# Optimization experiments

Hardware: AMD Instinct MI355X
Metric: run time of the kernel (lower is better)

## Reference

```python
import jax, jax.numpy as jnp
import numpy as np

EMBED_DIM = 1024
NUM_HEADS = 16
D_K = EMBED_DIM // NUM_HEADS


def setup_inputs() -> dict:
    key = jax.random.key(0)
    kx, kq, kk, kv, ko = jax.random.split(key, 5)
    scale = 1.0 / np.sqrt(EMBED_DIM)
    return {
        "x": jax.random.normal(kx, (4, 2048, EMBED_DIM), dtype=jnp.float32),
        # nn.Linear weights are [out, in]; we store them the same way.
        "w_q": jax.random.normal(kq, (EMBED_DIM, EMBED_DIM), dtype=jnp.float32) * scale,
        "w_k": jax.random.normal(kk, (EMBED_DIM, EMBED_DIM), dtype=jnp.float32) * scale,
        "w_v": jax.random.normal(kv, (EMBED_DIM, EMBED_DIM), dtype=jnp.float32) * scale,
        "w_o": jax.random.normal(ko, (EMBED_DIM, EMBED_DIM), dtype=jnp.float32) * scale,
    }


def reference(x, w_q, w_k, w_v, w_o):
    B, S, E = x.shape
    H, Dk = NUM_HEADS, D_K

    def proj(w):  # [B,S,E] @ [E,E]^T -> [B,H,S,Dk]
        y = jnp.einsum('bse,fe->bsf', x, w)
        return y.reshape(B, S, H, Dk).transpose(0, 2, 1, 3)

    q, k, v = proj(w_q), proj(w_k), proj(w_v)
    scores = jnp.einsum('bhsd,bhtd->bhst', q, k) / jnp.sqrt(jnp.float32(Dk))
    attn = jax.nn.softmax(scores, axis=-1)  # dropout p=0 -> identity
    out = jnp.einsum('bhst,bhtd->bhsd', attn, v)
    out = out.transpose(0, 2, 1, 3).reshape(B, S, E)
    return jnp.einsum('bse,fe->bsf', out, w_o)
```

## Files before the change

### kernel.cpp

```cpp
#include <hip/hip_runtime.h>
#include <stdint.h>

typedef unsigned short u16;
typedef __attribute__((ext_vector_type(8))) short bf16x8;
typedef __attribute__((ext_vector_type(4))) float f32x4;
typedef __attribute__((ext_vector_type(16))) float f32x16;

#define EMB 1024
#define SLEN 2048
#define NHD 16
#define DKH 64

__device__ __forceinline__ u16 f2bf(float f) {
  uint32_t u = __float_as_uint(f);
  u = (u + 0x7fffu + ((u >> 16) & 1u)) >> 16;
  return (u16)u;
}

__device__ __forceinline__ void load_lds16(const void* g, void* l) {
  __builtin_amdgcn_global_load_lds(
      (const __attribute__((address_space(1))) uint32_t*)g,
      (__attribute__((address_space(3))) uint32_t*)l, 16, 0, 0);
}

__global__ __launch_bounds__(256) void cvt_f32_bf16(const float* __restrict__ in,
                                                    u16* __restrict__ out, int n4) {
  int i = blockIdx.x * 256 + threadIdx.x;
  if (i >= n4) return;
  float4 v = ((const float4*)in)[i];
  union { u16 h[4]; uint64_t q; } o;
  o.h[0] = f2bf(v.x); o.h[1] = f2bf(v.y); o.h[2] = f2bf(v.z); o.h[3] = f2bf(v.w);
  ((uint64_t*)out)[i] = o.q;
}

__global__ __launch_bounds__(256) void cvt_w4(
    const float* __restrict__ w0, const float* __restrict__ w1,
    const float* __restrict__ w2, const float* __restrict__ w3,
    u16* __restrict__ o0, u16* __restrict__ o1,
    u16* __restrict__ o2, u16* __restrict__ o3) {
  const float* in = (blockIdx.y == 0) ? w0 : (blockIdx.y == 1) ? w1
                    : (blockIdx.y == 2) ? w2 : w3;
  u16* out = (blockIdx.y == 0) ? o0 : (blockIdx.y == 1) ? o1
             : (blockIdx.y == 2) ? o2 : o3;
  int i = blockIdx.x * 256 + threadIdx.x;
  float4 v = ((const float4*)in)[i];
  union { u16 h[4]; uint64_t q; } o;
  o.h[0] = f2bf(v.x); o.h[1] = f2bf(v.y); o.h[2] = f2bf(v.z); o.h[3] = f2bf(v.w);
  ((uint64_t*)out)[i] = o.q;
}

template<int MODE>
__device__ __forceinline__ void gemm_body(const u16* __restrict__ A,
                                          const u16* __restrict__ W,
                                          void* __restrict__ C,
                                          int bm, int bn,
                                          u16* At, u16* Bt) {
  const int tid = threadIdx.x;
  const int l = tid & 63, w = tid >> 6;
  const int wm = w >> 1, wn = w & 1;
  const int lr = l & 15, lg = l >> 4;

  f32x4 acc[4][4] = {};

  const int e0 = w * 1024 + l * 8;
  const int r0 = e0 >> 5, c0 = e0 & 31;
  const int e1 = e0 + 512;
  const int r1 = e1 >> 5, c1 = e1 & 31;
  const u16* Ag0 = A + (size_t)(bm + r0) * EMB + c0;
  const u16* Ag1 = A + (size_t)(bm + r1) * EMB + c1;
  const u16* Wg0 = W + (size_t)(bn + r0) * EMB + c0;
  const u16* Wg1 = W + (size_t)(bn + r1) * EMB + c1;

  auto stage = [&](int buf, int k0) {
    load_lds16(Ag0 + k0, At + buf * 4096 + w * 1024);
    load_lds16(Ag1 + k0, At + buf * 4096 + w * 1024 + 512);
    load_lds16(Wg0 + k0, Bt + buf * 4096 + w * 1024);
    load_lds16(Wg1 + k0, Bt + buf * 4096 + w * 1024 + 512);
  };

  stage(0, 0);
  stage(1, 32);
  int cur = 0;

#pragma unroll 1
  for (int it = 0; it < 32; ++it) {
    if (it < 31)
      asm volatile("s_waitcnt vmcnt(4)" ::: "memory");
    else
      asm volatile("s_waitcnt vmcnt(0)" ::: "memory");
    __builtin_amdgcn_s_barrier();
    if (it < 30) {
      int nb = cur + 2; if (nb >= 3) nb -= 3;
      stage(nb, (it + 2) * 32);
    }
    bf16x8 af[4], bf[4];
#pragma unroll
    for (int i = 0; i < 4; ++i)
      af[i] = *(const bf16x8*)(At + cur * 4096 + (wm * 64 + i * 16 + lr) * 32 + lg * 8);
#pragma unroll
    for (int j = 0; j < 4; ++j)
      bf[j] = *(const bf16x8*)(Bt + cur * 4096 + (wn * 64 + j * 16 + lr) * 32 + lg * 8);
    __builtin_amdgcn_s_setprio(1);
#pragma unroll
    for (int i = 0; i < 4; ++i)
#pragma unroll
      for (int j = 0; j < 4; ++j)
        acc[i][j] = __builtin_amdgcn_mfma_f32_16x16x32_bf16(af[i], bf[j], acc[i][j], 0, 0, 0);
    __builtin_amdgcn_s_setprio(0);
    ++cur; if (cur == 3) cur = 0;
  }

  if (MODE == 2) {
#pragma unroll
    for (int i = 0; i < 4; ++i) {
      const int m0 = bm + wm * 64 + i * 16 + lg * 4;
      const int bb = m0 >> 11;
      const int ss = m0 & 2047;
#pragma unroll
      for (int j = 0; j < 4; ++j) {
        const int n = bn + wn * 64 + j * 16 + lr;
        const int hh = n >> 6, dd = n & 63;
        union { u16 h[4]; uint64_t q; } pk;
#pragma unroll
        for (int r = 0; r < 4; ++r) pk.h[r] = f2bf(acc[i][j][r]);
        *(uint64_t*)((u16*)C + ((size_t)((bb * 16 + hh) * 64 + dd)) * 2048 + ss) = pk.q;
      }
    }
  } else {
#pragma unroll
    for (int i = 0; i < 4; ++i) {
      const int mb = bm + wm * 64 + i * 16 + lg * 4;
#pragma unroll
      for (int j = 0; j < 4; ++j) {
        const int col = bn + wn * 64 + j * 16 + lr;
#pragma unroll
        for (int r = 0; r < 4; ++r) {
          float v = acc[i][j][r];
          if (MODE == 1) v *= 0.18033688011112042f;
          if (MODE == 3)
            ((float*)C)[(size_t)(mb + r) * EMB + col] = v;
          else
            ((u16*)C)[(size_t)(mb + r) * EMB + col] = f2bf(v);
        }
      }
    }
  }
}

__global__ __launch_bounds__(256) void gemm_qkv(
    const u16* __restrict__ A,
    const u16* __restrict__ wq, const u16* __restrict__ wk, const u16* __restrict__ wv,
    u16* __restrict__ Qo, u16* __restrict__ Ko, u16* __restrict__ Vo) {
  __shared__ __align__(16) u16 At[3 * 4096];
  __shared__ __align__(16) u16 Bt[3 * 4096];
  const int bid = blockIdx.x;
  const int wgid = (bid & 7) * 192 + (bid >> 3);
  const int z = wgid >> 9;
  const int rem = wgid & 511;
  const int bm = (rem >> 3) * 128, bn = (rem & 7) * 128;
  if (z == 0) gemm_body<1>(A, wq, Qo, bm, bn, At, Bt);
  else if (z == 1) gemm_body<0>(A, wk, Ko, bm, bn, At, Bt);
  else gemm_body<2>(A, wv, Vo, bm, bn, At, Bt);
}

__global__ __launch_bounds__(256) void gemm_out(const u16* __restrict__ A,
                                                const u16* __restrict__ W,
                                                float* __restrict__ C) {
  __shared__ __align__(16) u16 At[3 * 4096];
  __shared__ __align__(16) u16 Bt[3 * 4096];
  const int bid = blockIdx.x;
  const int wgid = (bid & 7) * 64 + (bid >> 3);
  const int bm = (wgid >> 3) * 128, bn = (wgid & 7) * 128;
  gemm_body<3>(A, W, C, bm, bn, At, Bt);
}

__global__ __launch_bounds__(512, 4) void attn_fwd(const u16* __restrict__ Q,
                                                   const u16* __restrict__ K,
                                                   const u16* __restrict__ VT,
                                                   u16* __restrict__ O) {
  __shared__ __align__(16) u16 lds[3][2][64 * 64];
  const int tid = threadIdx.x;
  const int l = tid & 63, w = tid >> 6;
  const int ql = l & 31, hi = l >> 5;
  const int bid = blockIdx.x;
  const int bh = (bid & 7) * 8 + (bid >> 6);
  const int qt = (bid >> 3) & 7;
  const int b = bh >> 4, h = bh & 15;
  const int qw = qt * 256 + w * 32;
  const size_t qkb = ((size_t)b * SLEN) * EMB + h * DKH;
  const size_t vb = (size_t)bh * DKH * SLEN;

  const int srow = tid >> 3;
  const int scb = ((tid & 7) * 16) ^ ((srow & 7) << 4);
  const u16* Ksrc = K + qkb + (size_t)srow * EMB + (scb >> 1);
  const u16* Vsrc = VT + vb + (size_t)srow * SLEN + (scb >> 1);

  auto stage = [&](int buf, int t) {
    load_lds16(Ksrc + (size_t)t * 64 * EMB, (char*)(&lds[buf][0][0]) + w * 1024);
    load_lds16(Vsrc + t * 64, (char*)(&lds[buf][1][0]) + w * 1024);
  };

  bf16x8 qf[4];
#pragma unroll
  for (int ks = 0; ks < 4; ++ks)
    qf[ks] = *(const bf16x8*)(Q + qkb + (size_t)(qw + ql) * EMB + ks * 16 + hi * 8);

  f32x16 accd[2] = {};
  float lsum = 0.f;

  stage(0, 0);
  stage(1, 1);
  int cur = 0;
#pragma unroll 1
  for (int t = 0; t < 32; ++t) {
    if (t < 30) {
      int nb = cur + 2; if (nb >= 3) nb -= 3;
      stage(nb, t + 2);
      asm volatile("s_waitcnt vmcnt(4)" ::: "memory");
    } else if (t == 30) {
      asm volatile("s_waitcnt vmcnt(2)" ::: "memory");
    } else {
      asm volatile("s_waitcnt vmcnt(0)" ::: "memory");
    }
    __builtin_amdgcn_s_barrier();

    const u16* Kt = &lds[cur][0][0];
    const u16* Vt = &lds[cur][1][0];

    f32x16 sacc[2] = {};
    __builtin_amdgcn_s_setprio(1);
#pragma unroll
    for (int kf2 = 0; kf2 < 2; ++kf2) {
      const int row = kf2 * 32 + ql;
      const int swz = (row & 7) << 4;
#pragma unroll
      for (int ks = 0; ks < 4; ++ks) {
        bf16x8 kf = *(const bf16x8*)((const char*)Kt + row * 128 +
                                     ((ks * 32 + hi * 16) ^ swz));
        sacc[kf2] = __builtin_amdgcn_mfma_f32_32x32x16_bf16(kf, qf[ks], sacc[kf2], 0, 0, 0);
      }
    }
    __builtin_amdgcn_s_setprio(0);

#pragma unroll
    for (int kf2 = 0; kf2 < 2; ++kf2)
#pragma unroll
      for (int r = 0; r < 16; ++r)
        sacc[kf2][r] = __builtin_amdgcn_exp2f(sacc[kf2][r]);
    float ps[8];
#pragma unroll
    for (int g = 0; g < 8; ++g) {
      const int kf2 = g >> 2, r0 = (g & 3) * 4;
      ps[g] = (sacc[kf2][r0] + sacc[kf2][r0 + 1]) + (sacc[kf2][r0 + 2] + sacc[kf2][r0 + 3]);
    }
    lsum += ((ps[0] + ps[1]) + (ps[2] + ps[3])) + ((ps[4] + ps[5]) + (ps[6] + ps[7]));

    __builtin_amdgcn_s_setprio(1);
#pragma unroll
    for (int ks = 0; ks < 4; ++ks) {
      const int kf2 = ks >> 1;
      const int e0 = (ks & 1) * 8;
      uint32_t a0, a1, b0, b1;
      asm("v_cvt_pk_bf16_f32 %0, %1, %2" : "=v"(a0) : "v"(sacc[kf2][e0 + 0]), "v"(sacc[kf2][e0 + 1]));
      asm("v_cvt_pk_bf16_f32 %0, %1, %2" : "=v"(a1) : "v"(sacc[kf2][e0 + 2]), "v"(sacc[kf2][e0 + 3]));
      asm("v_cvt_pk_bf16_f32 %0, %1, %2" : "=v"(b0) : "v"(sacc[kf2][e0 + 4]), "v"(sacc[kf2][e0 + 5]));
      asm("v_cvt_pk_bf16_f32 %0, %1, %2" : "=v"(b1) : "v"(sacc[kf2][e0 + 6]), "v"(sacc[kf2][e0 + 7]));
      asm("v_permlane32_swap_b32 %0, %1" : "+v"(a0), "+v"(b0));
      asm("v_permlane32_swap_b32 %0, %1" : "+v"(a1), "+v"(b1));
      union { uint32_t d[4]; bf16x8 v; } pa;
      pa.d[0] = a0; pa.d[1] = a1; pa.d[2] = b0; pa.d[3] = b1;
#pragma unroll
      for (int df = 0; df < 2; ++df) {
        const int vr = df * 32 + ql;
        bf16x8 vf = *(const bf16x8*)((const char*)Vt + vr * 128 +
                                     ((ks * 32 + hi * 16) ^ ((vr & 7) << 4)));
        accd[df] = __builtin_amdgcn_mfma_f32_32x32x16_bf16(pa.v, vf, accd[df], 0, 0, 0);
      }
    }
    __builtin_amdgcn_s_setprio(0);
    __builtin_amdgcn_s_barrier();
    ++cur; if (cur == 3) cur = 0;
  }

  lsum += __shfl_xor(lsum, 32, 64);

  __syncthreads();
  u16* slice = &lds[0][0][0] + w * 2048;
#pragma unroll
  for (int reg = 0; reg < 16; ++reg) {
    const int rowq = (reg & 3) + 8 * (reg >> 2) + 4 * hi;
    const float li = 1.0f / __shfl(lsum, rowq, 64);
    slice[rowq * 64 + ql] = f2bf(accd[0][reg] * li);
    slice[rowq * 64 + 32 + ql] = f2bf(accd[1][reg] * li);
  }
  asm volatile("s_waitcnt lgkmcnt(0)" ::: "memory");
#pragma unroll
  for (int j = 0; j < 4; ++j) {
    const int byteoff = j * 1024 + l * 16;
    const int row = byteoff >> 7;
    const int colB = byteoff & 127;
    bf16x8 vv = *(const bf16x8*)((const char*)slice + byteoff);
    *(bf16x8*)(O + qkb + (size_t)(qw + row) * EMB + (colB >> 1)) = vv;
  }
}

extern "C" void kernel_launch(void* const* d_in, const int* in_sizes, int n_in,
                              void* d_out, int out_size, void* d_ws, size_t ws_size,
                              hipStream_t stream) {
  const float* x  = (const float*)d_in[0];
  const float* wq = (const float*)d_in[1];
  const float* wk = (const float*)d_in[2];
  const float* wv = (const float*)d_in[3];
  const float* wo = (const float*)d_in[4];

  char* ws = (char*)d_ws;
  u16* xb  = (u16*)(ws + 0);
  u16* wqb = (u16*)(ws + 16777216);
  u16* wkb = (u16*)(ws + 18874368);
  u16* wvb = (u16*)(ws + 20971520);
  u16* wob = (u16*)(ws + 23068672);
  u16* Qb  = (u16*)(ws + 25165824);
  u16* Kb  = (u16*)(ws + 41943040);
  u16* VTb = (u16*)(ws + 58720256);
  u16* AO  = (u16*)(ws + 75497472);

  cvt_f32_bf16<<<2097152 / 256, 256, 0, stream>>>(x, xb, 2097152);
  cvt_w4<<<dim3(262144 / 256, 4), 256, 0, stream>>>(wq, wk, wv, wo, wqb, wkb, wvb, wob);

  gemm_qkv<<<dim3(1536), 256, 0, stream>>>(xb, wqb, wkb, wvb, Qb, Kb, VTb);
  attn_fwd<<<dim3(512), 512, 0, stream>>>(Qb, Kb, VTb, AO);
  gemm_out<<<dim3(512), 256, 0, stream>>>(AO, wob, (float*)d_out);
}
```

Before: 178.3 us.

## Use 8 waves per GEMM tile and merge conversion kernels into one launch

The GEMM blocks grow from 256 to 512 threads. Each wave now computes a 64x32 sub-tile instead of 64x64, and the staging loads are split so each thread issues one A and one W load per stage. This halves the accumulator count per wave and doubles the number of waves available to hide latency, at the cost of less operand reuse per wave and more LDS reads in total. Separately, the x and weight fp32-to-bf16 conversions are fused into one kernel to drop a launch.

```diff
diff --git a/kernel.cpp b/kernel.cpp
--- a/kernel.cpp
+++ b/kernel.cpp
@@ -23,26 +23,25 @@
       (__attribute__((address_space(3))) uint32_t*)l, 16, 0, 0);
 }
 
-__global__ __launch_bounds__(256) void cvt_f32_bf16(const float* __restrict__ in,
-                                                    u16* __restrict__ out, int n4) {
-  int i = blockIdx.x * 256 + threadIdx.x;
-  if (i >= n4) return;
-  float4 v = ((const float4*)in)[i];
-  union { u16 h[4]; uint64_t q; } o;
-  o.h[0] = f2bf(v.x); o.h[1] = f2bf(v.y); o.h[2] = f2bf(v.z); o.h[3] = f2bf(v.w);
-  ((uint64_t*)out)[i] = o.q;
-}
-
-__global__ __launch_bounds__(256) void cvt_w4(
+__global__ __launch_bounds__(256) void cvt_all(
+    const float* __restrict__ x,
     const float* __restrict__ w0, const float* __restrict__ w1,
     const float* __restrict__ w2, const float* __restrict__ w3,
+    u16* __restrict__ xo,
     u16* __restrict__ o0, u16* __restrict__ o1,
     u16* __restrict__ o2, u16* __restrict__ o3) {
-  const float* in = (blockIdx.y == 0) ? w0 : (blockIdx.y == 1) ? w1
-                    : (blockIdx.y == 2) ? w2 : w3;
-  u16* out = (blockIdx.y == 0) ? o0 : (blockIdx.y == 1) ? o1
-             : (blockIdx.y == 2) ? o2 : o3;
-  int i = blockIdx.x * 256 + threadIdx.x;
+  const int bid = blockIdx.x;
+  const float* in;
+  u16* out;
+  int i;
+  if (bid < 8192) {
+    in = x; out = xo; i = bid * 256 + threadIdx.x;
+  } else {
+    const int ws = (bid - 8192) >> 10;
+    in  = (ws == 0) ? w0 : (ws == 1) ? w1 : (ws == 2) ? w2 : w3;
+    out = (ws == 0) ? o0 : (ws == 1) ? o1 : (ws == 2) ? o2 : o3;
+    i = ((bid - 8192) & 1023) * 256 + threadIdx.x;
+  }
   float4 v = ((const float4*)in)[i];
   union { u16 h[4]; uint64_t q; } o;
   o.h[0] = f2bf(v.x); o.h[1] = f2bf(v.y); o.h[2] = f2bf(v.z); o.h[3] = f2bf(v.w);
@@ -57,25 +56,19 @@
                                           u16* At, u16* Bt) {
   const int tid = threadIdx.x;
   const int l = tid & 63, w = tid >> 6;
-  const int wm = w >> 1, wn = w & 1;
+  const int wm = w >> 2, wn = w & 3;
   const int lr = l & 15, lg = l >> 4;
 
-  f32x4 acc[4][4] = {};
-
-  const int e0 = w * 1024 + l * 8;
-  const int r0 = e0 >> 5, c0 = e0 & 31;
-  const int e1 = e0 + 512;
-  const int r1 = e1 >> 5, c1 = e1 & 31;
-  const u16* Ag0 = A + (size_t)(bm + r0) * EMB + c0;
-  const u16* Ag1 = A + (size_t)(bm + r1) * EMB + c1;
-  const u16* Wg0 = W + (size_t)(bn + r0) * EMB + c0;
-  const u16* Wg1 = W + (size_t)(bn + r1) * EMB + c1;
+  f32x4 acc[4][2] = {};
+
+  const int sr = w * 16 + (l >> 2);
+  const int sc = (l & 3) * 8;
+  const u16* Ag = A + (size_t)(bm + sr) * EMB + sc;
+  const u16* Wg = W + (size_t)(bn + sr) * EMB + sc;
 
   auto stage = [&](int buf, int k0) {
-    load_lds16(Ag0 + k0, At + buf * 4096 + w * 1024);
-    load_lds16(Ag1 + k0, At + buf * 4096 + w * 1024 + 512);
-    load_lds16(Wg0 + k0, Bt + buf * 4096 + w * 1024);
-    load_lds16(Wg1 + k0, Bt + buf * 4096 + w * 1024 + 512);
+    load_lds16(Ag + k0, At + buf * 4096 + w * 512);
+    load_lds16(Wg + k0, Bt + buf * 4096 + w * 512);
   };
 
   stage(0, 0);
@@ -85,7 +78,7 @@
 #pragma unroll 1
   for (int it = 0; it < 32; ++it) {
     if (it < 31)
-      asm volatile("s_waitcnt vmcnt(4)" ::: "memory");
+      asm volatile("s_waitcnt vmcnt(2)" ::: "memory");
     else
       asm volatile("s_waitcnt vmcnt(0)" ::: "memory");
     __builtin_amdgcn_s_barrier();
@@ -93,18 +86,18 @@
       int nb = cur + 2; if (nb >= 3) nb -= 3;
       stage(nb, (it + 2) * 32);
     }
-    bf16x8 af[4], bf[4];
+    bf16x8 af[4], bf[2];
 #pragma unroll
     for (int i = 0; i < 4; ++i)
       af[i] = *(const bf16x8*)(At + cur * 4096 + (wm * 64 + i * 16 + lr) * 32 + lg * 8);
 #pragma unroll
-    for (int j = 0; j < 4; ++j)
-      bf[j] = *(const bf16x8*)(Bt + cur * 4096 + (wn * 64 + j * 16 + lr) * 32 + lg * 8);
+    for (int j = 0; j < 2; ++j)
+      bf[j] = *(const bf16x8*)(Bt + cur * 4096 + (wn * 32 + j * 16 + lr) * 32 + lg * 8);
     __builtin_amdgcn_s_setprio(1);
 #pragma unroll
     for (int i = 0; i < 4; ++i)
 #pragma unroll
-      for (int j = 0; j < 4; ++j)
+      for (int j = 0; j < 2; ++j)
         acc[i][j] = __builtin_amdgcn_mfma_f32_16x16x32_bf16(af[i], bf[j], acc[i][j], 0, 0, 0);
     __builtin_amdgcn_s_setprio(0);
     ++cur; if (cur == 3) cur = 0;
@@ -117,8 +110,8 @@
       const int bb = m0 >> 11;
       const int ss = m0 & 2047;
 #pragma unroll
-      for (int j = 0; j < 4; ++j) {
-        const int n = bn + wn * 64 + j * 16 + lr;
+      for (int j = 0; j < 2; ++j) {
+        const int n = bn + wn * 32 + j * 16 + lr;
         const int hh = n >> 6, dd = n & 63;
         union { u16 h[4]; uint64_t q; } pk;
 #pragma unroll
@@ -131,8 +124,8 @@
     for (int i = 0; i < 4; ++i) {
       const int mb = bm + wm * 64 + i * 16 + lg * 4;
 #pragma unroll
-      for (int j = 0; j < 4; ++j) {
-        const int col = bn + wn * 64 + j * 16 + lr;
+      for (int j = 0; j < 2; ++j) {
+        const int col = bn + wn * 32 + j * 16 + lr;
 #pragma unroll
         for (int r = 0; r < 4; ++r) {
           float v = acc[i][j][r];
@@ -147,7 +140,7 @@
   }
 }
 
-__global__ __launch_bounds__(256) void gemm_qkv(
+__global__ __launch_bounds__(512) void gemm_qkv(
     const u16* __restrict__ A,
     const u16* __restrict__ wq, const u16* __restrict__ wk, const u16* __restrict__ wv,
     u16* __restrict__ Qo, u16* __restrict__ Ko, u16* __restrict__ Vo) {
@@ -163,7 +156,7 @@
   else gemm_body<2>(A, wv, Vo, bm, bn, At, Bt);
 }
 
-__global__ __launch_bounds__(256) void gemm_out(const u16* __restrict__ A,
+__global__ __launch_bounds__(512) void gemm_out(const u16* __restrict__ A,
                                                 const u16* __restrict__ W,
                                                 float* __restrict__ C) {
   __shared__ __align__(16) u16 At[3 * 4096];
@@ -324,10 +317,9 @@
   u16* VTb = (u16*)(ws + 58720256);
   u16* AO  = (u16*)(ws + 75497472);
 
-  cvt_f32_bf16<<<2097152 / 256, 256, 0, stream>>>(x, xb, 2097152);
-  cvt_w4<<<dim3(262144 / 256, 4), 256, 0, stream>>>(wq, wk, wv, wo, wqb, wkb, wvb, wob);
-
-  gemm_qkv<<<dim3(1536), 256, 0, stream>>>(xb, wqb, wkb, wvb, Qb, Kb, VTb);
+  cvt_all<<<dim3(12288), 256, 0, stream>>>(x, wq, wk, wv, wo, xb, wqb, wkb, wvb, wob);
+
+  gemm_qkv<<<dim3(1536), 512, 0, stream>>>(xb, wqb, wkb, wvb, Qb, Kb, VTb);
   attn_fwd<<<dim3(512), 512, 0, stream>>>(Qb, Kb, VTb, AO);
-  gemm_out<<<dim3(512), 256, 0, stream>>>(AO, wob, (float*)d_out);
-}
+  gemm_out<<<dim3(512), 512, 0, stream>>>(AO, wob, (float*)d_out);
+}
```

Result: slower. 181.8 us (+2.0%).
